# Performance work log

Hardware: AMD Instinct MI355X
Metric: run time of the kernel (lower is better)

## Reference

```python
import jax, jax.numpy as jnp
import numpy as np

E, D, I, T = 8, 4096, 1024, 32768  # experts, model dim, dim//4, total packed tokens


def setup_inputs() -> dict:
    key = jax.random.key(0)
    k1, k2, k3, k4 = jax.random.split(key, 4)
    x = jax.random.normal(k1, (T, D), dtype=jnp.float32)
    # trunc_normal(std=0.02) approximated by scaled normal for the reference
    w1 = jax.random.normal(k2, (E, D, I), dtype=jnp.float32) * 0.02
    w2 = jax.random.normal(k3, (E, I, D), dtype=jnp.float32) * 0.02
    w3 = jax.random.normal(k4, (E, D, I), dtype=jnp.float32) * 0.02
    # tokens split evenly across experts; sum == T
    num_tokens_per_expert = jnp.full((E,), T // E, dtype=jnp.int32)
    return {"x": x, "w1": w1, "w2": w2, "w3": w3,
            "num_tokens_per_expert": num_tokens_per_expert}


def reference(x, w1, w2, w3, num_tokens_per_expert):
    # bf16 compute, cast back to input dtype (matches ops.gmm path in torch code)
    g = num_tokens_per_expert.astype(jnp.int32)
    xb = x.astype(jnp.bfloat16)
    w1b = w1.astype(jnp.bfloat16)
    w2b = w2.astype(jnp.bfloat16)
    w3b = w3.astype(jnp.bfloat16)
    # grouped GEMM: rows of x are grouped by expert per g
    x1 = jax.lax.ragged_dot(xb, w1b, g)          # [T, I]
    x3 = jax.lax.ragged_dot(xb, w3b, g)          # [T, I]
    h = jax.nn.silu(x1) * x3                      # SwiGLU
    out = jax.lax.ragged_dot(h, w2b, g)           # [T, D]
    return out.astype(x.dtype)
```

## Files before the change

kernel.cpp:

```cpp
#include <hip/hip_runtime.h>
#include <hip/hip_bf16.h>

typedef __attribute__((ext_vector_type(8))) short bf16x8;
typedef __attribute__((ext_vector_type(4))) float f32x4;

#define SBAR() __builtin_amdgcn_sched_barrier(0)
#define WBAR() __builtin_amdgcn_s_barrier()

template<int N> __device__ __forceinline__ void vmcw() {
  if constexpr (N >= 12)     asm volatile("s_waitcnt vmcnt(12)" ::: "memory");
  else if constexpr (N == 8) asm volatile("s_waitcnt vmcnt(8)" ::: "memory");
  else if constexpr (N == 4) asm volatile("s_waitcnt vmcnt(4)" ::: "memory");
  else                       asm volatile("s_waitcnt vmcnt(0)" ::: "memory");
}

__device__ __forceinline__ ushort f2bf(float f) {
  union { float f; unsigned u; } v; v.f = f;
  unsigned r = v.u + 0x7fffu + ((v.u >> 16) & 1u);
  return (ushort)(r >> 16);
}

__device__ __forceinline__ void gld_lds16(const ushort* gsrc, ushort* lds) {
  __builtin_amdgcn_global_load_lds((const __attribute__((address_space(1))) void*)gsrc,
                                   (__attribute__((address_space(3))) void*)lds, 16, 0, 0);
}

__device__ __forceinline__ f32x4 MF(bf16x8 a, bf16x8 b, f32x4 c) {
  return __builtin_amdgcn_mfma_f32_16x16x32_bf16(a, b, c, 0, 0, 0);
}

__device__ __forceinline__ void xcd_map(int bid, int CT, int& r, int& c) {
  const int xcd = bid & 7, j = bid >> 3;
  r = xcd + 8 * (j / CT);
  c = j % CT;
}

__device__ __forceinline__ int expert_of(const int* g, int E, int m0) {
  int e = 0, base = 0;
  while (e < E - 1 && m0 >= base + g[e]) { base += g[e]; ++e; }
  return e;
}

__global__ __launch_bounds__(256) void k_pack_x(
    const float* __restrict__ x, ushort* __restrict__ xb, int D) {
  __shared__ ushort sm[256][66];
  const int kt = blockIdx.x;
  const int rt = blockIdx.y;
  const int t = threadIdx.x;
  const int c0 = kt * 64;
  const size_t r0 = (size_t)rt * 256;
#pragma unroll
  for (int p = 0; p < 16; ++p) {
    const int row = p * 16 + (t >> 4);
    const float4 v = *reinterpret_cast<const float4*>(x + (r0 + row) * D + c0 + (t & 15) * 4);
    ushort4 u; u.x = f2bf(v.x); u.y = f2bf(v.y); u.z = f2bf(v.z); u.w = f2bf(v.w);
    *reinterpret_cast<ushort4*>(&sm[row][(t & 15) * 4]) = u;
  }
  __syncthreads();
  ushort* outp = xb + ((size_t)rt * (D >> 6) + kt) * 16384;
#pragma unroll
  for (int p = 0; p < 8; ++p) {
    ushort u[8];
#pragma unroll
    for (int j = 0; j < 8; ++j) u[j] = sm[t][p * 8 + j];
    *reinterpret_cast<uint4*>(outp + p * 2048 + t * 8) = *reinterpret_cast<uint4*>(u);
  }
}

__global__ __launch_bounds__(256) void k_pack_w13(
    const float* __restrict__ w1, const float* __restrict__ w3,
    ushort* __restrict__ w1p, ushort* __restrict__ w3p, int R, int C) {
  __shared__ ushort sm[64][66];
  const int bz = blockIdx.z;
  const int e = bz >> 1;
  const size_t mat = (size_t)R * C;
  const float* s = ((bz & 1) ? w3 : w1) + (size_t)e * mat;
  ushort* d = ((bz & 1) ? w3p : w1p) + (size_t)e * mat;
  const int c0 = blockIdx.x * 64;
  const int r0 = blockIdx.y * 64;
  const int t = threadIdx.x;
#pragma unroll
  for (int p = 0; p < 4; ++p) {
    const int r = p * 16 + (t >> 4);
    const float4 v = *reinterpret_cast<const float4*>(s + (size_t)(r0 + r) * C + c0 + (t & 15) * 4);
    ushort4 u; u.x = f2bf(v.x); u.y = f2bf(v.y); u.z = f2bf(v.z); u.w = f2bf(v.w);
    *reinterpret_cast<ushort4*>(&sm[r][(t & 15) * 4]) = u;
  }
  __syncthreads();
  const size_t tilebase = ((size_t)(c0 >> 7) * (R >> 6) + (r0 >> 6)) * 8192;
  const int nbase = c0 & 127;
#pragma unroll
  for (int p = 0; p < 2; ++p) {
    const int uu = p * 256 + t;
    const int kc = uu >> 6;
    const int rr = uu & 63;
    ushort u[8];
#pragma unroll
    for (int j = 0; j < 8; ++j) u[j] = sm[kc * 8 + j][rr];
    *reinterpret_cast<uint4*>(d + tilebase + (size_t)kc * 1024 + (size_t)(nbase + rr) * 8) =
        *reinterpret_cast<uint4*>(u);
  }
}

__global__ __launch_bounds__(256) void k_pack_w2(
    const float* __restrict__ w, ushort* __restrict__ wp, int R, int C) {
  __shared__ ushort sm[64][66];
  const int e = blockIdx.z;
  const size_t mat = (size_t)R * C;
  const float* s = w + (size_t)e * mat;
  ushort* d = wp + (size_t)e * mat;
  const int c0 = blockIdx.x * 64;
  const int r0 = blockIdx.y * 64;
  const int t = threadIdx.x;
#pragma unroll
  for (int p = 0; p < 4; ++p) {
    const int r = p * 16 + (t >> 4);
    const float4 v = *reinterpret_cast<const float4*>(s + (size_t)(r0 + r) * C + c0 + (t & 15) * 4);
    ushort4 u; u.x = f2bf(v.x); u.y = f2bf(v.y); u.z = f2bf(v.z); u.w = f2bf(v.w);
    *reinterpret_cast<ushort4*>(&sm[r][(t & 15) * 4]) = u;
  }
  __syncthreads();
  const size_t tilebase = ((size_t)(c0 >> 8) * (R >> 6) + (r0 >> 6)) * 16384;
  const int nbase = c0 & 255;
#pragma unroll
  for (int p = 0; p < 2; ++p) {
    const int uu = p * 256 + t;
    const int kc = uu >> 6;
    const int rr = uu & 63;
    ushort u[8];
#pragma unroll
    for (int j = 0; j < 8; ++j) u[j] = sm[kc * 8 + j][rr];
    *reinterpret_cast<uint4*>(d + tilebase + (size_t)kc * 2048 + (size_t)(nbase + rr) * 8) =
        *reinterpret_cast<uint4*>(u);
  }
}

template<bool PF, int C1, int C2>
__device__ __forceinline__ void g1_tile(
    ushort* B, const ushort* nA, const ushort* nB1, const ushort* nB3,
    int sto, int aoff, int b1off, int b3off,
    f32x4 (&acc1)[8][2], f32x4 (&acc3)[8][2]) {
  bf16x8 af[4], b1f[2], b3f[2];
  SBAR();
#pragma unroll
  for (int mi = 0; mi < 4; ++mi) af[mi] = *(const bf16x8*)&B[aoff + mi * 128];
  b1f[0] = *(const bf16x8*)&B[b1off];       b1f[1] = *(const bf16x8*)&B[b1off + 128];
  b3f[0] = *(const bf16x8*)&B[b3off];       b3f[1] = *(const bf16x8*)&B[b3off + 128];
  SBAR(); WBAR(); SBAR();
  __builtin_amdgcn_s_setprio(1);
#pragma unroll
  for (int mi = 0; mi < 4; ++mi)
#pragma unroll
    for (int ni = 0; ni < 2; ++ni) {
      acc1[mi][ni] = MF(af[mi], b1f[ni], acc1[mi][ni]);
      acc3[mi][ni] = MF(af[mi], b3f[ni], acc3[mi][ni]);
    }
  __builtin_amdgcn_s_setprio(0);
  SBAR(); WBAR();
  SBAR();
#pragma unroll
  for (int mi = 0; mi < 4; ++mi) af[mi] = *(const bf16x8*)&B[aoff + (mi + 4) * 128];
  SBAR(); WBAR(); SBAR();
  if (PF) {
    gld_lds16(nA + sto,         B + sto);
    gld_lds16(nA + 4096 + sto,  B + 4096 + sto);
    gld_lds16(nB1 + sto,        B + 16384 + sto);
    gld_lds16(nB3 + sto,        B + 24576 + sto);
  }
  __builtin_amdgcn_s_setprio(1);
#pragma unroll
  for (int mi = 0; mi < 4; ++mi)
#pragma unroll
    for (int ni = 0; ni < 2; ++ni) {
      acc1[mi + 4][ni] = MF(af[mi], b1f[ni], acc1[mi + 4][ni]);
      acc3[mi + 4][ni] = MF(af[mi], b3f[ni], acc3[mi + 4][ni]);
    }
  __builtin_amdgcn_s_setprio(0);
  SBAR();
  vmcw<C1>();
  WBAR();
  SBAR();
#pragma unroll
  for (int mi = 0; mi < 4; ++mi) af[mi] = *(const bf16x8*)&B[aoff + 8192 + mi * 128];
  b1f[0] = *(const bf16x8*)&B[b1off + 4096]; b1f[1] = *(const bf16x8*)&B[b1off + 4096 + 128];
  b3f[0] = *(const bf16x8*)&B[b3off + 4096]; b3f[1] = *(const bf16x8*)&B[b3off + 4096 + 128];
  SBAR(); WBAR(); SBAR();
  __builtin_amdgcn_s_setprio(1);
#pragma unroll
  for (int mi = 0; mi < 4; ++mi)
#pragma unroll
    for (int ni = 0; ni < 2; ++ni) {
      acc1[mi][ni] = MF(af[mi], b1f[ni], acc1[mi][ni]);
      acc3[mi][ni] = MF(af[mi], b3f[ni], acc3[mi][ni]);
    }
  __builtin_amdgcn_s_setprio(0);
  SBAR(); WBAR();
  SBAR();
#pragma unroll
  for (int mi = 0; mi < 4; ++mi) af[mi] = *(const bf16x8*)&B[aoff + 8192 + (mi + 4) * 128];
  SBAR(); WBAR(); SBAR();
  if (PF) {
    gld_lds16(nA + 8192 + sto,   B + 8192 + sto);
    gld_lds16(nA + 12288 + sto,  B + 12288 + sto);
    gld_lds16(nB1 + 4096 + sto,  B + 20480 + sto);
    gld_lds16(nB3 + 4096 + sto,  B + 28672 + sto);
  }
  __builtin_amdgcn_s_setprio(1);
#pragma unroll
  for (int mi = 0; mi < 4; ++mi)
#pragma unroll
    for (int ni = 0; ni < 2; ++ni) {
      acc1[mi + 4][ni] = MF(af[mi], b1f[ni], acc1[mi + 4][ni]);
      acc3[mi + 4][ni] = MF(af[mi], b3f[ni], acc3[mi + 4][ni]);
    }
  __builtin_amdgcn_s_setprio(0);
  SBAR();
  vmcw<C2>();
  WBAR();
}

__global__ __launch_bounds__(512, 2) void k_gemm1_8p(
    const ushort* __restrict__ xb, const ushort* __restrict__ w1p,
    const ushort* __restrict__ w3p, const int* __restrict__ g,
    ushort* __restrict__ h, int T, int D, int I, int E) {
  __shared__ ushort lds[2][32768];

  const int CT = I >> 7;
  int r, c; xcd_map(blockIdx.x, CT, r, c);
  const int m0 = r << 8, n0 = c << 7;
  const int e = expert_of(g, E, m0);

  const int tid = threadIdx.x;
  const int lane = tid & 63, wave = tid >> 6;
  const int wr = wave >> 2, wc = wave & 3;
  const int l15 = lane & 15, l16 = lane >> 4;

  const int KT = D >> 6;
  const ushort* pA  = xb  + (size_t)r * (D >> 6) * 16384;
  const ushort* pB1 = w1p + (size_t)e * I * D + (size_t)c * (D >> 6) * 8192;
  const ushort* pB3 = w3p + (size_t)e * I * D + (size_t)c * (D >> 6) * 8192;

  const int sto = tid * 8;
  const int aoff  = l16 * 2048 + (wr * 128 + l15) * 8;
  const int b1off = 16384 + l16 * 1024 + (wc * 32 + l15) * 8;
  const int b3off = b1off + 8192;

  const f32x4 zero = {0.f, 0.f, 0.f, 0.f};
  f32x4 acc1[8][2], acc3[8][2];
#pragma unroll
  for (int mi = 0; mi < 8; ++mi)
#pragma unroll
    for (int ni = 0; ni < 2; ++ni) { acc1[mi][ni] = zero; acc3[mi][ni] = zero; }

  {
    ushort* L0 = lds[0]; ushort* L1 = lds[1];
    gld_lds16(pA + sto,          L0 + sto);
    gld_lds16(pA + 4096 + sto,   L0 + 4096 + sto);
    gld_lds16(pB1 + sto,         L0 + 16384 + sto);
    gld_lds16(pB3 + sto,         L0 + 24576 + sto);
    gld_lds16(pA + 8192 + sto,   L0 + 8192 + sto);
    gld_lds16(pA + 12288 + sto,  L0 + 12288 + sto);
    gld_lds16(pB1 + 4096 + sto,  L0 + 20480 + sto);
    gld_lds16(pB3 + 4096 + sto,  L0 + 28672 + sto);
    gld_lds16(pA + 16384 + sto,         L1 + sto);
    gld_lds16(pA + 16384 + 4096 + sto,  L1 + 4096 + sto);
    gld_lds16(pB1 + 8192 + sto,         L1 + 16384 + sto);
    gld_lds16(pB3 + 8192 + sto,         L1 + 24576 + sto);
    gld_lds16(pA + 16384 + 8192 + sto,  L1 + 8192 + sto);
    gld_lds16(pA + 16384 + 12288 + sto, L1 + 12288 + sto);
    gld_lds16(pB1 + 8192 + 4096 + sto,  L1 + 20480 + sto);
    gld_lds16(pB3 + 8192 + 4096 + sto,  L1 + 28672 + sto);
  }
  vmcw<12>(); WBAR(); SBAR();

  int t = 0;
  for (; t < KT - 2; ++t)
    g1_tile<true, 12, 12>(lds[t & 1], pA + (size_t)(t + 2) * 16384,
                          pB1 + (size_t)(t + 2) * 8192, pB3 + (size_t)(t + 2) * 8192,
                          sto, aoff, b1off, b3off, acc1, acc3);
  g1_tile<false, 8, 4>(lds[t & 1], pA, pB1, pB3, sto, aoff, b1off, b3off, acc1, acc3);
  ++t;
  g1_tile<false, 0, 0>(lds[t & 1], pA, pB1, pB3, sto, aoff, b1off, b3off, acc1, acc3);

#pragma unroll
  for (int mi = 0; mi < 8; ++mi)
#pragma unroll
    for (int ni = 0; ni < 2; ++ni)
#pragma unroll
      for (int rr = 0; rr < 4; ++rr) {
        const float v1 = acc1[mi][ni][rr];
        const float v3 = acc3[mi][ni][rr];
        const float sv = v1 / (1.f + __expf(-v1));
        const int row = m0 + wr * 128 + mi * 16 + l16 * 4 + rr;
        const int col = n0 + wc * 32 + ni * 16 + l15;
        const size_t off = ((size_t)(row >> 8) * (I >> 6) + (col >> 6)) * 16384 +
                           ((col >> 3) & 7) * 2048 + (row & 255) * 8 + (col & 7);
        h[off] = f2bf(sv * v3);
      }
}

template<bool PF, int C1, int C2>
__device__ __forceinline__ void g2_tile(
    ushort* B, const ushort* nA, const ushort* nB,
    int sto, int aoff, int boff, f32x4 (&acc)[8][4]) {
  bf16x8 af[4], bf[4];
  SBAR();
#pragma unroll
  for (int mi = 0; mi < 4; ++mi) af[mi] = *(const bf16x8*)&B[aoff + mi * 128];
#pragma unroll
  for (int ni = 0; ni < 4; ++ni) bf[ni] = *(const bf16x8*)&B[boff + ni * 128];
  SBAR(); WBAR(); SBAR();
  __builtin_amdgcn_s_setprio(1);
#pragma unroll
  for (int mi = 0; mi < 4; ++mi)
#pragma unroll
    for (int ni = 0; ni < 4; ++ni) acc[mi][ni] = MF(af[mi], bf[ni], acc[mi][ni]);
  __builtin_amdgcn_s_setprio(0);
  SBAR(); WBAR();
  SBAR();
#pragma unroll
  for (int mi = 0; mi < 4; ++mi) af[mi] = *(const bf16x8*)&B[aoff + (mi + 4) * 128];
  SBAR(); WBAR(); SBAR();
  if (PF) {
    gld_lds16(nA + sto,         B + sto);
    gld_lds16(nA + 4096 + sto,  B + 4096 + sto);
    gld_lds16(nB + sto,         B + 16384 + sto);
    gld_lds16(nB + 4096 + sto,  B + 20480 + sto);
  }
  __builtin_amdgcn_s_setprio(1);
#pragma unroll
  for (int mi = 0; mi < 4; ++mi)
#pragma unroll
    for (int ni = 0; ni < 4; ++ni) acc[mi + 4][ni] = MF(af[mi], bf[ni], acc[mi + 4][ni]);
  __builtin_amdgcn_s_setprio(0);
  SBAR();
  vmcw<C1>();
  WBAR();
  SBAR();
#pragma unroll
  for (int mi = 0; mi < 4; ++mi) af[mi] = *(const bf16x8*)&B[aoff + 8192 + mi * 128];
#pragma unroll
  for (int ni = 0; ni < 4; ++ni) bf[ni] = *(const bf16x8*)&B[boff + 8192 + ni * 128];
  SBAR(); WBAR(); SBAR();
  __builtin_amdgcn_s_setprio(1);
#pragma unroll
  for (int mi = 0; mi < 4; ++mi)
#pragma unroll
    for (int ni = 0; ni < 4; ++ni) acc[mi][ni] = MF(af[mi], bf[ni], acc[mi][ni]);
  __builtin_amdgcn_s_setprio(0);
  SBAR(); WBAR();
  SBAR();
#pragma unroll
  for (int mi = 0; mi < 4; ++mi) af[mi] = *(const bf16x8*)&B[aoff + 8192 + (mi + 4) * 128];
  SBAR(); WBAR(); SBAR();
  if (PF) {
    gld_lds16(nA + 8192 + sto,   B + 8192 + sto);
    gld_lds16(nA + 12288 + sto,  B + 12288 + sto);
    gld_lds16(nB + 8192 + sto,   B + 24576 + sto);
    gld_lds16(nB + 12288 + sto,  B + 28672 + sto);
  }
  __builtin_amdgcn_s_setprio(1);
#pragma unroll
  for (int mi = 0; mi < 4; ++mi)
#pragma unroll
    for (int ni = 0; ni < 4; ++ni) acc[mi + 4][ni] = MF(af[mi], bf[ni], acc[mi + 4][ni]);
  __builtin_amdgcn_s_setprio(0);
  SBAR();
  vmcw<C2>();
  WBAR();
}

__global__ __launch_bounds__(512, 2) void k_gemm2_8p(
    const ushort* __restrict__ h, const ushort* __restrict__ w2p,
    const int* __restrict__ g, float* __restrict__ out,
    int T, int D, int I, int E) {
  __shared__ ushort lds[2][32768];

  const int CT = D >> 8;
  int r, cb; xcd_map(blockIdx.x, CT, r, cb);
  const int m0 = r << 8, n0 = cb << 8;
  const int e = expert_of(g, E, m0);

  const int tid = threadIdx.x;
  const int lane = tid & 63, wave = tid >> 6;
  const int wr = wave >> 2, wc = wave & 3;
  const int l15 = lane & 15, l16 = lane >> 4;

  const int KT = I >> 6;
  const ushort* pA = h   + (size_t)r * (I >> 6) * 16384;
  const ushort* pB = w2p + (size_t)e * D * I + (size_t)cb * (I >> 6) * 16384;

  const int sto = tid * 8;
  const int aoff = l16 * 2048 + (wr * 128 + l15) * 8;
  const int boff = 16384 + l16 * 2048 + (wc * 64 + l15) * 8;

  const f32x4 zero = {0.f, 0.f, 0.f, 0.f};
  f32x4 acc[8][4];
#pragma unroll
  for (int mi = 0; mi < 8; ++mi)
#pragma unroll
    for (int ni = 0; ni < 4; ++ni) acc[mi][ni] = zero;

  {
    ushort* L0 = lds[0]; ushort* L1 = lds[1];
    gld_lds16(pA + sto,          L0 + sto);
    gld_lds16(pA + 4096 + sto,   L0 + 4096 + sto);
    gld_lds16(pB + sto,          L0 + 16384 + sto);
    gld_lds16(pB + 4096 + sto,   L0 + 20480 + sto);
    gld_lds16(pA + 8192 + sto,   L0 + 8192 + sto);
    gld_lds16(pA + 12288 + sto,  L0 + 12288 + sto);
    gld_lds16(pB + 8192 + sto,   L0 + 24576 + sto);
    gld_lds16(pB + 12288 + sto,  L0 + 28672 + sto);
    gld_lds16(pA + 16384 + sto,          L1 + sto);
    gld_lds16(pA + 16384 + 4096 + sto,   L1 + 4096 + sto);
    gld_lds16(pB + 16384 + sto,          L1 + 16384 + sto);
    gld_lds16(pB + 16384 + 4096 + sto,   L1 + 20480 + sto);
    gld_lds16(pA + 16384 + 8192 + sto,   L1 + 8192 + sto);
    gld_lds16(pA + 16384 + 12288 + sto,  L1 + 12288 + sto);
    gld_lds16(pB + 16384 + 8192 + sto,   L1 + 24576 + sto);
    gld_lds16(pB + 16384 + 12288 + sto,  L1 + 28672 + sto);
  }
  vmcw<12>(); WBAR(); SBAR();

  int t = 0;
  for (; t < KT - 2; ++t)
    g2_tile<true, 12, 12>(lds[t & 1], pA + (size_t)(t + 2) * 16384,
                          pB + (size_t)(t + 2) * 16384, sto, aoff, boff, acc);
  g2_tile<false, 8, 4>(lds[t & 1], pA, pB, sto, aoff, boff, acc);
  ++t;
  g2_tile<false, 0, 0>(lds[t & 1], pA, pB, sto, aoff, boff, acc);

#pragma unroll
  for (int mi = 0; mi < 8; ++mi)
#pragma unroll
    for (int ni = 0; ni < 4; ++ni)
#pragma unroll
      for (int rr = 0; rr < 4; ++rr) {
        const int row = m0 + wr * 128 + mi * 16 + l16 * 4 + rr;
        const int col = n0 + wc * 64 + ni * 16 + l15;
        out[(size_t)row * D + col] = acc[mi][ni][rr];
      }
}

extern "C" void kernel_launch(void* const* d_in, const int* in_sizes, int n_in,
                              void* d_out, int out_size, void* d_ws, size_t ws_size,
                              hipStream_t stream) {
  const float* x  = (const float*)d_in[0];
  const float* w1 = (const float*)d_in[1];
  const float* w2 = (const float*)d_in[2];
  const float* w3 = (const float*)d_in[3];
  const int*   g  = (const int*)d_in[4];

  const int E = in_sizes[4];
  const int D = 4096;
  const int I = 1024;
  const int T = in_sizes[0] / D;

  const size_t szW = (size_t)E * D * I * sizeof(ushort);
  const size_t szH = (size_t)T * I * sizeof(ushort);
  const size_t szX = (size_t)T * D * sizeof(ushort);
  const size_t need = 2 * szW + szH + szX;
  if (ws_size < need) return;

  char* ws = (char*)d_ws;
  ushort* w1p = (ushort*)ws;
  ushort* w3p = (ushort*)(ws + szW);
  ushort* h   = (ushort*)(ws + 2 * szW);
  ushort* xb  = (ushort*)(ws + 2 * szW + szH);
  ushort* w2p = w1p;

  float* out = (float*)d_out;

  k_pack_w13<<<dim3(I / 64, D / 64, 2 * E), 256, 0, stream>>>(w1, w3, w1p, w3p, D, I);
  k_pack_x<<<dim3(D / 64, T / 256), 256, 0, stream>>>(x, xb, D);

  k_gemm1_8p<<<dim3((T / 256) * (I / 128)), 512, 0, stream>>>(xb, w1p, w3p, g, h, T, D, I, E);

  k_pack_w2<<<dim3(D / 64, I / 64, E), 256, 0, stream>>>(w2, w2p, I, D);

  k_gemm2_8p<<<dim3((T / 256) * (D / 256)), 512, 0, stream>>>(h, w2p, g, out, T, D, I, E);
}
```

Baseline: 1.052 ms.

## Switch GEMM mainloops to 3-stage ring of K=32 tiles with one barrier

Both grouped GEMM kernels now step K in 32-wide slices through a three-slot LDS ring instead of double-buffered 64-wide tiles. Prefetch of slice t+2 is issued at the start of each step and followed by a single barrier, replacing the many sub-step barriers per tile. The aim is to cut barrier and scheduling overhead and overlap loads more evenly. In exchange there are twice as many loop iterations, fewer MFMAs between waits, and LDS drops from 128KB to 96KB per block.

```diff
diff --git a/kernel.cpp b/kernel.cpp
--- a/kernel.cpp
+++ b/kernel.cpp
@@ -8,9 +8,7 @@
 #define WBAR() __builtin_amdgcn_s_barrier()
 
 template<int N> __device__ __forceinline__ void vmcw() {
-  if constexpr (N >= 12)     asm volatile("s_waitcnt vmcnt(12)" ::: "memory");
-  else if constexpr (N == 8) asm volatile("s_waitcnt vmcnt(8)" ::: "memory");
-  else if constexpr (N == 4) asm volatile("s_waitcnt vmcnt(4)" ::: "memory");
+  if constexpr (N == 4)      asm volatile("s_waitcnt vmcnt(4)" ::: "memory");
   else                       asm volatile("s_waitcnt vmcnt(0)" ::: "memory");
 }
 
@@ -135,87 +133,35 @@
   }
 }
 
-template<bool PF, int C1, int C2>
-__device__ __forceinline__ void g1_tile(
-    ushort* B, const ushort* nA, const ushort* nB1, const ushort* nB3,
+template<bool PF, int C>
+__device__ __forceinline__ void g1_tile32(
+    const ushort* cur, ushort* stg,
+    const ushort* sA, const ushort* sB1, const ushort* sB3,
     int sto, int aoff, int b1off, int b3off,
     f32x4 (&acc1)[8][2], f32x4 (&acc3)[8][2]) {
-  bf16x8 af[4], b1f[2], b3f[2];
   SBAR();
-#pragma unroll
-  for (int mi = 0; mi < 4; ++mi) af[mi] = *(const bf16x8*)&B[aoff + mi * 128];
-  b1f[0] = *(const bf16x8*)&B[b1off];       b1f[1] = *(const bf16x8*)&B[b1off + 128];
-  b3f[0] = *(const bf16x8*)&B[b3off];       b3f[1] = *(const bf16x8*)&B[b3off + 128];
-  SBAR(); WBAR(); SBAR();
+  if (PF) {
+    gld_lds16(sA + sto,        stg + sto);
+    gld_lds16(sA + 4096 + sto, stg + 4096 + sto);
+    gld_lds16(sB1 + sto,       stg + 8192 + sto);
+    gld_lds16(sB3 + sto,       stg + 12288 + sto);
+  }
+  SBAR();
+  bf16x8 af[8], b1f[2], b3f[2];
+#pragma unroll
+  for (int mi = 0; mi < 8; ++mi) af[mi] = *(const bf16x8*)&cur[aoff + mi * 128];
+  b1f[0] = *(const bf16x8*)&cur[b1off];       b1f[1] = *(const bf16x8*)&cur[b1off + 128];
+  b3f[0] = *(const bf16x8*)&cur[b3off];       b3f[1] = *(const bf16x8*)&cur[b3off + 128];
   __builtin_amdgcn_s_setprio(1);
 #pragma unroll
-  for (int mi = 0; mi < 4; ++mi)
+  for (int mi = 0; mi < 8; ++mi)
 #pragma unroll
     for (int ni = 0; ni < 2; ++ni) {
       acc1[mi][ni] = MF(af[mi], b1f[ni], acc1[mi][ni]);
       acc3[mi][ni] = MF(af[mi], b3f[ni], acc3[mi][ni]);
     }
   __builtin_amdgcn_s_setprio(0);
-  SBAR(); WBAR();
-  SBAR();
-#pragma unroll
-  for (int mi = 0; mi < 4; ++mi) af[mi] = *(const bf16x8*)&B[aoff + (mi + 4) * 128];
-  SBAR(); WBAR(); SBAR();
-  if (PF) {
-    gld_lds16(nA + sto,         B + sto);
-    gld_lds16(nA + 4096 + sto,  B + 4096 + sto);
-    gld_lds16(nB1 + sto,        B + 16384 + sto);
-    gld_lds16(nB3 + sto,        B + 24576 + sto);
-  }
-  __builtin_amdgcn_s_setprio(1);
-#pragma unroll
-  for (int mi = 0; mi < 4; ++mi)
-#pragma unroll
-    for (int ni = 0; ni < 2; ++ni) {
-      acc1[mi + 4][ni] = MF(af[mi], b1f[ni], acc1[mi + 4][ni]);
-      acc3[mi + 4][ni] = MF(af[mi], b3f[ni], acc3[mi + 4][ni]);
-    }
-  __builtin_amdgcn_s_setprio(0);
-  SBAR();
-  vmcw<C1>();
-  WBAR();
-  SBAR();
-#pragma unroll
-  for (int mi = 0; mi < 4; ++mi) af[mi] = *(const bf16x8*)&B[aoff + 8192 + mi * 128];
-  b1f[0] = *(const bf16x8*)&B[b1off + 4096]; b1f[1] = *(const bf16x8*)&B[b1off + 4096 + 128];
-  b3f[0] = *(const bf16x8*)&B[b3off + 4096]; b3f[1] = *(const bf16x8*)&B[b3off + 4096 + 128];
-  SBAR(); WBAR(); SBAR();
-  __builtin_amdgcn_s_setprio(1);
-#pragma unroll
-  for (int mi = 0; mi < 4; ++mi)
-#pragma unroll
-    for (int ni = 0; ni < 2; ++ni) {
-      acc1[mi][ni] = MF(af[mi], b1f[ni], acc1[mi][ni]);
-      acc3[mi][ni] = MF(af[mi], b3f[ni], acc3[mi][ni]);
-    }
-  __builtin_amdgcn_s_setprio(0);
-  SBAR(); WBAR();
-  SBAR();
-#pragma unroll
-  for (int mi = 0; mi < 4; ++mi) af[mi] = *(const bf16x8*)&B[aoff + 8192 + (mi + 4) * 128];
-  SBAR(); WBAR(); SBAR();
-  if (PF) {
-    gld_lds16(nA + 8192 + sto,   B + 8192 + sto);
-    gld_lds16(nA + 12288 + sto,  B + 12288 + sto);
-    gld_lds16(nB1 + 4096 + sto,  B + 20480 + sto);
-    gld_lds16(nB3 + 4096 + sto,  B + 28672 + sto);
-  }
-  __builtin_amdgcn_s_setprio(1);
-#pragma unroll
-  for (int mi = 0; mi < 4; ++mi)
-#pragma unroll
-    for (int ni = 0; ni < 2; ++ni) {
-      acc1[mi + 4][ni] = MF(af[mi], b1f[ni], acc1[mi + 4][ni]);
-      acc3[mi + 4][ni] = MF(af[mi], b3f[ni], acc3[mi + 4][ni]);
-    }
-  __builtin_amdgcn_s_setprio(0);
-  SBAR();
-  vmcw<C2>();
+  vmcw<C>();
   WBAR();
 }
 
@@ -223,7 +169,7 @@
     const ushort* __restrict__ xb, const ushort* __restrict__ w1p,
     const ushort* __restrict__ w3p, const int* __restrict__ g,
     ushort* __restrict__ h, int T, int D, int I, int E) {
-  __shared__ ushort lds[2][32768];
+  __shared__ ushort lds[3 * 16384];
 
   const int CT = I >> 7;
   int r, c; xcd_map(blockIdx.x, CT, r, c);
@@ -235,15 +181,15 @@
   const int wr = wave >> 2, wc = wave & 3;
   const int l15 = lane & 15, l16 = lane >> 4;
 
-  const int KT = D >> 6;
+  const int KT = D >> 5;
   const ushort* pA  = xb  + (size_t)r * (D >> 6) * 16384;
   const ushort* pB1 = w1p + (size_t)e * I * D + (size_t)c * (D >> 6) * 8192;
   const ushort* pB3 = w3p + (size_t)e * I * D + (size_t)c * (D >> 6) * 8192;
 
   const int sto = tid * 8;
   const int aoff  = l16 * 2048 + (wr * 128 + l15) * 8;
-  const int b1off = 16384 + l16 * 1024 + (wc * 32 + l15) * 8;
-  const int b3off = b1off + 8192;
+  const int b1off = 8192 + l16 * 1024 + (wc * 32 + l15) * 8;
+  const int b3off = b1off + 4096;
 
   const f32x4 zero = {0.f, 0.f, 0.f, 0.f};
   f32x4 acc1[8][2], acc3[8][2];
@@ -253,34 +199,33 @@
     for (int ni = 0; ni < 2; ++ni) { acc1[mi][ni] = zero; acc3[mi][ni] = zero; }
 
   {
-    ushort* L0 = lds[0]; ushort* L1 = lds[1];
+    ushort* L0 = lds; ushort* L1 = lds + 16384;
     gld_lds16(pA + sto,          L0 + sto);
     gld_lds16(pA + 4096 + sto,   L0 + 4096 + sto);
-    gld_lds16(pB1 + sto,         L0 + 16384 + sto);
-    gld_lds16(pB3 + sto,         L0 + 24576 + sto);
-    gld_lds16(pA + 8192 + sto,   L0 + 8192 + sto);
-    gld_lds16(pA + 12288 + sto,  L0 + 12288 + sto);
-    gld_lds16(pB1 + 4096 + sto,  L0 + 20480 + sto);
-    gld_lds16(pB3 + 4096 + sto,  L0 + 28672 + sto);
-    gld_lds16(pA + 16384 + sto,         L1 + sto);
-    gld_lds16(pA + 16384 + 4096 + sto,  L1 + 4096 + sto);
-    gld_lds16(pB1 + 8192 + sto,         L1 + 16384 + sto);
-    gld_lds16(pB3 + 8192 + sto,         L1 + 24576 + sto);
-    gld_lds16(pA + 16384 + 8192 + sto,  L1 + 8192 + sto);
-    gld_lds16(pA + 16384 + 12288 + sto, L1 + 12288 + sto);
-    gld_lds16(pB1 + 8192 + 4096 + sto,  L1 + 20480 + sto);
-    gld_lds16(pB3 + 8192 + 4096 + sto,  L1 + 28672 + sto);
-  }
-  vmcw<12>(); WBAR(); SBAR();
-
-  int t = 0;
-  for (; t < KT - 2; ++t)
-    g1_tile<true, 12, 12>(lds[t & 1], pA + (size_t)(t + 2) * 16384,
-                          pB1 + (size_t)(t + 2) * 8192, pB3 + (size_t)(t + 2) * 8192,
-                          sto, aoff, b1off, b3off, acc1, acc3);
-  g1_tile<false, 8, 4>(lds[t & 1], pA, pB1, pB3, sto, aoff, b1off, b3off, acc1, acc3);
-  ++t;
-  g1_tile<false, 0, 0>(lds[t & 1], pA, pB1, pB3, sto, aoff, b1off, b3off, acc1, acc3);
+    gld_lds16(pB1 + sto,         L0 + 8192 + sto);
+    gld_lds16(pB3 + sto,         L0 + 12288 + sto);
+    gld_lds16(pA + 8192 + sto,   L1 + sto);
+    gld_lds16(pA + 12288 + sto,  L1 + 4096 + sto);
+    gld_lds16(pB1 + 4096 + sto,  L1 + 8192 + sto);
+    gld_lds16(pB3 + 4096 + sto,  L1 + 12288 + sto);
+  }
+  vmcw<4>(); WBAR();
+
+  const ushort* sA  = pA  + 2 * 8192;
+  const ushort* sB1 = pB1 + 2 * 4096;
+  const ushort* sB3 = pB3 + 2 * 4096;
+  int curo = 0, stgo = 2 * 16384;
+
+  for (int t = 0; t < KT - 2; ++t) {
+    g1_tile32<true, 4>(lds + curo, lds + stgo, sA, sB1, sB3,
+                       sto, aoff, b1off, b3off, acc1, acc3);
+    sA += 8192; sB1 += 4096; sB3 += 4096;
+    curo = (curo == 32768) ? 0 : curo + 16384;
+    stgo = (stgo == 32768) ? 0 : stgo + 16384;
+  }
+  g1_tile32<false, 0>(lds + curo, lds, sA, sB1, sB3, sto, aoff, b1off, b3off, acc1, acc3);
+  curo = (curo == 32768) ? 0 : curo + 16384;
+  g1_tile32<false, 0>(lds + curo, lds, sA, sB1, sB3, sto, aoff, b1off, b3off, acc1, acc3);
 
 #pragma unroll
   for (int mi = 0; mi < 8; ++mi)
@@ -299,74 +244,31 @@
       }
 }
 
-template<bool PF, int C1, int C2>
-__device__ __forceinline__ void g2_tile(
-    ushort* B, const ushort* nA, const ushort* nB,
+template<bool PF, int C>
+__device__ __forceinline__ void g2_tile32(
+    const ushort* cur, ushort* stg,
+    const ushort* sA, const ushort* sB,
     int sto, int aoff, int boff, f32x4 (&acc)[8][4]) {
-  bf16x8 af[4], bf[4];
   SBAR();
-#pragma unroll
-  for (int mi = 0; mi < 4; ++mi) af[mi] = *(const bf16x8*)&B[aoff + mi * 128];
-#pragma unroll
-  for (int ni = 0; ni < 4; ++ni) bf[ni] = *(const bf16x8*)&B[boff + ni * 128];
-  SBAR(); WBAR(); SBAR();
+  if (PF) {
+    gld_lds16(sA + sto,        stg + sto);
+    gld_lds16(sA + 4096 + sto, stg + 4096 + sto);
+    gld_lds16(sB + sto,        stg + 8192 + sto);
+    gld_lds16(sB + 4096 + sto, stg + 12288 + sto);
+  }
+  SBAR();
+  bf16x8 af[8], bf[4];
+#pragma unroll
+  for (int mi = 0; mi < 8; ++mi) af[mi] = *(const bf16x8*)&cur[aoff + mi * 128];
+#pragma unroll
+  for (int ni = 0; ni < 4; ++ni) bf[ni] = *(const bf16x8*)&cur[boff + ni * 128];
   __builtin_amdgcn_s_setprio(1);
 #pragma unroll
-  for (int mi = 0; mi < 4; ++mi)
+  for (int mi = 0; mi < 8; ++mi)
 #pragma unroll
     for (int ni = 0; ni < 4; ++ni) acc[mi][ni] = MF(af[mi], bf[ni], acc[mi][ni]);
   __builtin_amdgcn_s_setprio(0);
-  SBAR(); WBAR();
-  SBAR();
-#pragma unroll
-  for (int mi = 0; mi < 4; ++mi) af[mi] = *(const bf16x8*)&B[aoff + (mi + 4) * 128];
-  SBAR(); WBAR(); SBAR();
-  if (PF) {
-    gld_lds16(nA + sto,         B + sto);
-    gld_lds16(nA + 4096 + sto,  B + 4096 + sto);
-    gld_lds16(nB + sto,         B + 16384 + sto);
-    gld_lds16(nB + 4096 + sto,  B + 20480 + sto);
-  }
-  __builtin_amdgcn_s_setprio(1);
-#pragma unroll
-  for (int mi = 0; mi < 4; ++mi)
-#pragma unroll
-    for (int ni = 0; ni < 4; ++ni) acc[mi + 4][ni] = MF(af[mi], bf[ni], acc[mi + 4][ni]);
-  __builtin_amdgcn_s_setprio(0);
-  SBAR();
-  vmcw<C1>();
-  WBAR();
-  SBAR();
-#pragma unroll
-  for (int mi = 0; mi < 4; ++mi) af[mi] = *(const bf16x8*)&B[aoff + 8192 + mi * 128];
-#pragma unroll
-  for (int ni = 0; ni < 4; ++ni) bf[ni] = *(const bf16x8*)&B[boff + 8192 + ni * 128];
-  SBAR(); WBAR(); SBAR();
-  __builtin_amdgcn_s_setprio(1);
-#pragma unroll
-  for (int mi = 0; mi < 4; ++mi)
-#pragma unroll
-    for (int ni = 0; ni < 4; ++ni) acc[mi][ni] = MF(af[mi], bf[ni], acc[mi][ni]);
-  __builtin_amdgcn_s_setprio(0);
-  SBAR(); WBAR();
-  SBAR();
-#pragma unroll
-  for (int mi = 0; mi < 4; ++mi) af[mi] = *(const bf16x8*)&B[aoff + 8192 + (mi + 4) * 128];
-  SBAR(); WBAR(); SBAR();
-  if (PF) {
-    gld_lds16(nA + 8192 + sto,   B + 8192 + sto);
-    gld_lds16(nA + 12288 + sto,  B + 12288 + sto);
-    gld_lds16(nB + 8192 + sto,   B + 24576 + sto);
-    gld_lds16(nB + 12288 + sto,  B + 28672 + sto);
-  }
-  __builtin_amdgcn_s_setprio(1);
-#pragma unroll
-  for (int mi = 0; mi < 4; ++mi)
-#pragma unroll
-    for (int ni = 0; ni < 4; ++ni) acc[mi + 4][ni] = MF(af[mi], bf[ni], acc[mi + 4][ni]);
-  __builtin_amdgcn_s_setprio(0);
-  SBAR();
-  vmcw<C2>();
+  vmcw<C>();
   WBAR();
 }
 
@@ -374,7 +276,7 @@
     const ushort* __restrict__ h, const ushort* __restrict__ w2p,
     const int* __restrict__ g, float* __restrict__ out,
     int T, int D, int I, int E) {
-  __shared__ ushort lds[2][32768];
+  __shared__ ushort lds[3 * 16384];
 
   const int CT = D >> 8;
   int r, cb; xcd_map(blockIdx.x, CT, r, cb);
@@ -386,13 +288,13 @@
   const int wr = wave >> 2, wc = wave & 3;
   const int l15 = lane & 15, l16 = lane >> 4;
 
-  const int KT = I >> 6;
+  const int KT = I >> 5;
   const ushort* pA = h   + (size_t)r * (I >> 6) * 16384;
   const ushort* pB = w2p + (size_t)e * D * I + (size_t)cb * (I >> 6) * 16384;
 
   const int sto = tid * 8;
   const int aoff = l16 * 2048 + (wr * 128 + l15) * 8;
-  const int boff = 16384 + l16 * 2048 + (wc * 64 + l15) * 8;
+  const int boff = 8192 + l16 * 2048 + (wc * 64 + l15) * 8;
 
   const f32x4 zero = {0.f, 0.f, 0.f, 0.f};
   f32x4 acc[8][4];
@@ -402,33 +304,31 @@
     for (int ni = 0; ni < 4; ++ni) acc[mi][ni] = zero;
 
   {
-    ushort* L0 = lds[0]; ushort* L1 = lds[1];
+    ushort* L0 = lds; ushort* L1 = lds + 16384;
     gld_lds16(pA + sto,          L0 + sto);
     gld_lds16(pA + 4096 + sto,   L0 + 4096 + sto);
-    gld_lds16(pB + sto,          L0 + 16384 + sto);
-    gld_lds16(pB + 4096 + sto,   L0 + 20480 + sto);
-    gld_lds16(pA + 8192 + sto,   L0 + 8192 + sto);
-    gld_lds16(pA + 12288 + sto,  L0 + 12288 + sto);
-    gld_lds16(pB + 8192 + sto,   L0 + 24576 + sto);
-    gld_lds16(pB + 12288 + sto,  L0 + 28672 + sto);
-    gld_lds16(pA + 16384 + sto,          L1 + sto);
-    gld_lds16(pA + 16384 + 4096 + sto,   L1 + 4096 + sto);
-    gld_lds16(pB + 16384 + sto,          L1 + 16384 + sto);
-    gld_lds16(pB + 16384 + 4096 + sto,   L1 + 20480 + sto);
-    gld_lds16(pA + 16384 + 8192 + sto,   L1 + 8192 + sto);
-    gld_lds16(pA + 16384 + 12288 + sto,  L1 + 12288 + sto);
-    gld_lds16(pB + 16384 + 8192 + sto,   L1 + 24576 + sto);
-    gld_lds16(pB + 16384 + 12288 + sto,  L1 + 28672 + sto);
-  }
-  vmcw<12>(); WBAR(); SBAR();
-
-  int t = 0;
-  for (; t < KT - 2; ++t)
-    g2_tile<true, 12, 12>(lds[t & 1], pA + (size_t)(t + 2) * 16384,
-                          pB + (size_t)(t + 2) * 16384, sto, aoff, boff, acc);
-  g2_tile<false, 8, 4>(lds[t & 1], pA, pB, sto, aoff, boff, acc);
-  ++t;
-  g2_tile<false, 0, 0>(lds[t & 1], pA, pB, sto, aoff, boff, acc);
+    gld_lds16(pB + sto,          L0 + 8192 + sto);
+    gld_lds16(pB + 4096 + sto,   L0 + 12288 + sto);
+    gld_lds16(pA + 8192 + sto,   L1 + sto);
+    gld_lds16(pA + 12288 + sto,  L1 + 4096 + sto);
+    gld_lds16(pB + 8192 + sto,   L1 + 8192 + sto);
+    gld_lds16(pB + 12288 + sto,  L1 + 12288 + sto);
+  }
+  vmcw<4>(); WBAR();
+
+  const ushort* sA = pA + 2 * 8192;
+  const ushort* sB = pB + 2 * 8192;
+  int curo = 0, stgo = 2 * 16384;
+
+  for (int t = 0; t < KT - 2; ++t) {
+    g2_tile32<true, 4>(lds + curo, lds + stgo, sA, sB, sto, aoff, boff, acc);
+    sA += 8192; sB += 8192;
+    curo = (curo == 32768) ? 0 : curo + 16384;
+    stgo = (stgo == 32768) ? 0 : stgo + 16384;
+  }
+  g2_tile32<false, 0>(lds + curo, lds, sA, sB, sto, aoff, boff, acc);
+  curo = (curo == 32768) ? 0 : curo + 16384;
+  g2_tile32<false, 0>(lds + curo, lds, sA, sB, sto, aoff, boff, acc);
 
 #pragma unroll
   for (int mi = 0; mi < 8; ++mi)
```

New measurement: 1.048 ms (median of 2 runs). Within noise of the previous version (-0.4%).
